# Kernel tuning notes

Measured on AMD Instinct MI355X. Metric: run time of the kernel, lower is better.

The kernel has to match this reference:

```python
import jax, jax.numpy as jnp
import numpy as np

B, S, D, H = 8, 577, 768, 12
P, KW = 576, 32            # num_patches, num_wormholes
HD = D // H                # head_dim = 64
SCALE = HD ** -0.5
TEMP = 0.1
GRID = 24                  # sqrt(P)
CANTOR_W = 0.3


def _cantor_position_bias():
    idx = np.arange(P)
    xg, yg = idx % GRID, idx // GRID
    s = xg + yg
    z = (s * (s + 1) // 2 + yg).astype(np.float32)
    fp = z / max(z.max(), 1.0)
    aff = 1.0 - np.abs(fp[None, :] - fp[:, None])
    np.fill_diagonal(aff, -1e9)
    return jnp.asarray(aff * CANTOR_W, dtype=jnp.float32)


def setup_inputs() -> dict:
    key = jax.random.key(0)
    ks = jax.random.split(key, 12)
    MLP = 4 * D
    w = lambda k, sh: jax.random.normal(k, sh, dtype=jnp.float32) * 0.02
    return {
        "x": jax.random.normal(ks[0], (B, S, D), dtype=jnp.float32),
        "g1": jnp.ones((D,), jnp.float32), "b1": jnp.zeros((D,), jnp.float32),
        "wq": w(ks[1], (D, D)), "bq": jnp.zeros((D,), jnp.float32),
        "wk": w(ks[2], (D, D)), "bk": jnp.zeros((D,), jnp.float32),
        "pos_bias": _cantor_position_bias(),
        "w_qkv": w(ks[3], (D, 3 * D)), "b_qkv": jnp.zeros((3 * D,), jnp.float32),
        "w_proj": w(ks[4], (D, D)), "b_proj": jnp.zeros((D,), jnp.float32),
        "g2": jnp.ones((D,), jnp.float32), "b2": jnp.zeros((D,), jnp.float32),
        "w_mlp1": w(ks[5], (D, 4 * D)), "b_mlp1": jnp.zeros((4 * D,), jnp.float32),
        "w_mlp2": w(ks[6], (4 * D, D)), "b_mlp2": jnp.zeros((D,), jnp.float32),
    }


def _ln(x, g, b):
    m = x.mean(-1, keepdims=True)
    v = x.var(-1, keepdims=True)
    return (x - m) / jnp.sqrt(v + 1e-5) * g + b


def _l2norm(x):  # F.normalize(dim=-1)
    return x / jnp.maximum(jnp.linalg.norm(x, axis=-1, keepdims=True), 1e-12)


def reference(x, g1, b1, wq, bq, wk, bk, pos_bias, w_qkv, b_qkv,
              w_proj, b_proj, g2, b2, w_mlp1, b_mlp1, w_mlp2, b_mlp2):
    xn = _ln(x, g1, b1)

    # --- learned wormhole router (content top-k) ---
    xp = xn[:, 1:, :]                                     # [B,P,D]
    q = _l2norm(xp @ wq + bq)
    k = _l2norm(xp @ wk + bk)
    scores = jnp.einsum('bpd,bqd->bpq', q, k) + pos_bias  # [B,P,P]
    scores = jnp.where(jnp.eye(P, dtype=bool), -1e9, scores) / TEMP
    topk_scores, routes = jax.lax.top_k(scores, KW)       # [B,P,K]
    weights = jax.nn.softmax(topk_scores, axis=-1)

    # --- qkv ---
    qkv = (xn @ w_qkv + b_qkv).reshape(B, S, 3, H, HD).transpose(2, 0, 3, 1, 4)
    Q, Kf, V = qkv[0], qkv[1], qkv[2]                     # [B,H,S,HD]

    # --- CLS: dense attention over all tokens ---
    attn_cls = jax.nn.softmax(jnp.einsum('bhqd,bhkd->bhqk', Q[:, :, :1], Kf) * SCALE, -1)
    out_cls = jnp.einsum('bhqk,bhkd->bhqd', attn_cls, V)  # [B,H,1,HD]

    # --- patches: sparse attention over gathered wormhole K/V ---
    Qp, Kp, Vp = Q[:, :, 1:], Kf[:, :, 1:], V[:, :, 1:]   # [B,H,P,HD]
    bi = jnp.arange(B)[:, None, None, None]
    hi = jnp.arange(H)[None, :, None, None]
    ri = routes[:, None, :, :]                            # [B,1,P,K] -> bcast [B,H,P,K]
    Kg = Kp[bi, hi, ri]                                   # [B,H,P,K,HD]
    Vg = Vp[bi, hi, ri]
    sp = jnp.einsum('bhpd,bhpkd->bhpk', Qp, Kg) * SCALE
    sp = sp + jnp.maximum(jnp.log(weights), -10.0)[:, None]
    ap = jax.nn.softmax(sp, axis=-1)
    out_p = jnp.einsum('bhpk,bhpkd->bhpd', ap, Vg)        # [B,H,P,HD]

    out = jnp.concatenate([out_cls, out_p], axis=2)       # [B,H,S,HD]
    out = out.transpose(0, 2, 1, 3).reshape(B, S, D)
    x = x + (out @ w_proj + b_proj)

    # --- MLP ---
    h = jax.nn.gelu(_ln(x, g2, b2) @ w_mlp1 + b_mlp1, approximate=False)
    x = x + (h @ w_mlp2 + b_mlp2)
    return x
```

## Files before the change

### kernel.cpp

```cpp
#include <hip/hip_runtime.h>
#include <math.h>

#define B_  8
#define S_  577
#define D_  768
#define H_  12
#define P_  576
#define KW_ 32
#define HD_ 64
constexpr int   MS       = B_ * S_;
constexpr int   MP       = B_ * P_;
constexpr float SCALE_   = 0.125f;
constexpr float INV_TEMP = 10.0f;

typedef __attribute__((ext_vector_type(8))) short bf16x8;
typedef __attribute__((ext_vector_type(4))) float f32x4;

__device__ __forceinline__ unsigned short f2bf(float f) {
  unsigned int x = __float_as_uint(f);
  x += 0x7fffu + ((x >> 16) & 1u);
  return (unsigned short)(x >> 16);
}
__device__ __forceinline__ float bf2f(unsigned short h) {
  return __uint_as_float((unsigned int)h << 16);
}
__device__ __forceinline__ void gl_lds16(const unsigned short* g,
                                         unsigned short* l) {
  __builtin_amdgcn_global_load_lds(
      (const __attribute__((address_space(1))) void*)g,
      (__attribute__((address_space(3))) void*)l, 16, 0, 0);
}
__device__ __forceinline__ void unpack8(bf16x8 v, float* f) {
  union { bf16x8 v8; unsigned int w[4]; } u;
  u.v8 = v;
#pragma unroll
  for (int i = 0; i < 4; ++i) {
    f[2 * i]     = __uint_as_float(u.w[i] << 16);
    f[2 * i + 1] = __uint_as_float(u.w[i] & 0xffff0000u);
  }
}
__device__ __forceinline__ int xcd_swz(int orig, int nwg) {
  const int q = nwg >> 3, r = nwg & 7;
  const int xcd = orig & 7, idx = orig >> 3;
  const int start = (xcd < r) ? xcd * (q + 1) : r * (q + 1) + (xcd - r) * q;
  return start + idx;
}

template <bool LO>
__global__ __launch_bounds__(256) void ln_rows_bf(
    const float* __restrict__ X, const float* __restrict__ g,
    const float* __restrict__ bta, unsigned short* __restrict__ Yh,
    unsigned short* __restrict__ Yl) {
  const int r = blockIdx.x, tid = threadIdx.x;
  const float* row = X + (long)r * D_;
  float v[3];
  float s = 0.f, sq = 0.f;
#pragma unroll
  for (int t = 0; t < 3; ++t) {
    v[t] = row[tid + t * 256];
    s += v[t];
    sq = fmaf(v[t], v[t], sq);
  }
#pragma unroll
  for (int off = 32; off; off >>= 1) {
    s  += __shfl_xor(s, off);
    sq += __shfl_xor(sq, off);
  }
  __shared__ float rs[4], rq[4];
  if ((tid & 63) == 0) { rs[tid >> 6] = s; rq[tid >> 6] = sq; }
  __syncthreads();
  s  = rs[0] + rs[1] + rs[2] + rs[3];
  sq = rq[0] + rq[1] + rq[2] + rq[3];
  const float m   = s * (1.f / D_);
  const float var = sq * (1.f / D_) - m * m;
  const float inv = rsqrtf(var + 1e-5f);
#pragma unroll
  for (int t = 0; t < 3; ++t) {
    const int c = tid + t * 256;
    const float y = (v[t] - m) * inv * g[c] + bta[c];
    const unsigned short h = f2bf(y);
    Yh[(long)r * D_ + c] = h;
    if (LO) Yl[(long)r * D_ + c] = f2bf(y - bf2f(h));
  }
}

__global__ __launch_bounds__(256) void l2norm_hl(
    const float* __restrict__ X, unsigned short* __restrict__ Yh,
    unsigned short* __restrict__ Yl) {
  const int r = blockIdx.x, tid = threadIdx.x;
  const float* row = X + (long)r * D_;
  float v[3];
  float sq = 0.f;
#pragma unroll
  for (int t = 0; t < 3; ++t) {
    v[t] = row[tid + t * 256];
    sq = fmaf(v[t], v[t], sq);
  }
#pragma unroll
  for (int off = 32; off; off >>= 1) sq += __shfl_xor(sq, off);
  __shared__ float rq[4];
  if ((tid & 63) == 0) rq[tid >> 6] = sq;
  __syncthreads();
  sq = rq[0] + rq[1] + rq[2] + rq[3];
  const float sc = 1.f / fmaxf(sqrtf(sq), 1e-12f);
#pragma unroll
  for (int t = 0; t < 3; ++t) {
    const float y = v[t] * sc;
    const unsigned short h = f2bf(y);
    Yh[(long)r * D_ + tid + t * 256] = h;
    Yl[(long)r * D_ + tid + t * 256] = f2bf(y - bf2f(h));
  }
}

__global__ __launch_bounds__(256) void transpose_hl(
    const float* __restrict__ W, unsigned short* __restrict__ Th,
    unsigned short* __restrict__ Tl, int K, int N, int rowoff) {
  __shared__ float t[32][33];
  const int tx = threadIdx.x & 31, ty = threadIdx.x >> 5;
  const int n0 = blockIdx.x * 32, k0 = blockIdx.y * 32;
#pragma unroll
  for (int i = ty; i < 32; i += 8)
    t[i][tx] = W[(long)(k0 + i) * N + n0 + tx];
  __syncthreads();
#pragma unroll
  for (int i = ty; i < 32; i += 8) {
    const float w = t[tx][i];
    const unsigned short h = f2bf(w);
    const long o = (long)(rowoff + n0 + i) * K + k0 + tx;
    Th[o] = h;
    if (Tl) Tl[o] = f2bf(w - bf2f(h));
  }
}

enum { BEPI_QKV = 0, BEPI_ADD = 1, BEPI_GELU = 2 };

template <int EPI>
__global__ __launch_bounds__(256, 3) void gemm_bf16(
    const unsigned short* __restrict__ A, const unsigned short* __restrict__ Wt,
    const float* __restrict__ bias, const float* __restrict__ R,
    float* __restrict__ C, unsigned short* __restrict__ Cbf,
    int M, int N, int K,
    unsigned short* __restrict__ Qb, unsigned short* __restrict__ Kb,
    unsigned short* __restrict__ Vb) {
  constexpr int BK = 64;
  __shared__ __align__(16) unsigned short ldsA[128 * BK];
  __shared__ __align__(16) unsigned short ldsB[128 * BK];
  const int tid = threadIdx.x, wave = tid >> 6, lane = tid & 63;
  const int wr = wave >> 1, wc = wave & 1;
  const int l16 = lane & 15, l4 = lane >> 4;
  const int NB = N >> 7;
  const int wgid = xcd_swz(blockIdx.x, gridDim.x);
  const int bm = wgid / NB, bn = wgid - bm * NB;
  const int row0 = bm * 128;

  f32x4 acc[4][4];
#pragma unroll
  for (int i = 0; i < 4; ++i)
#pragma unroll
    for (int j = 0; j < 4; ++j) acc[i][j] = (f32x4){0.f, 0.f, 0.f, 0.f};

  const unsigned short* ga[4];
  const unsigned short* gb[4];
#pragma unroll
  for (int t = 0; t < 4; ++t) {
    const int c = tid + (t << 8);
    const int r = c >> 3, p = c & 7, s = p ^ (r & 7);
    int ar = row0 + r; if (ar > M - 1) ar = M - 1;
    ga[t] = A + (long)ar * K + (s << 3);
    gb[t] = Wt + (long)(bn * 128 + r) * K + (s << 3);
  }

  for (int k0 = 0; k0 < K; k0 += BK) {
    __syncthreads();
#pragma unroll
    for (int t = 0; t < 4; ++t) {
      gl_lds16(ga[t] + k0, ldsA + ((tid + (t << 8)) << 3));
      gl_lds16(gb[t] + k0, ldsB + ((tid + (t << 8)) << 3));
    }
    __syncthreads();
#pragma unroll
    for (int sub = 0; sub < 2; ++sub) {
      bf16x8 af[4], bfr[4];
#pragma unroll
      for (int i = 0; i < 4; ++i) {
        const int row = wr * 64 + i * 16 + l16;
        const int pos = ((sub << 2) + l4) ^ (row & 7);
        af[i] = *(const bf16x8*)(ldsA + row * BK + (pos << 3));
      }
#pragma unroll
      for (int j = 0; j < 4; ++j) {
        const int row = wc * 64 + j * 16 + l16;
        const int pos = ((sub << 2) + l4) ^ (row & 7);
        bfr[j] = *(const bf16x8*)(ldsB + row * BK + (pos << 3));
      }
#pragma unroll
      for (int i = 0; i < 4; ++i)
#pragma unroll
        for (int j = 0; j < 4; ++j)
          acc[i][j] = __builtin_amdgcn_mfma_f32_16x16x32_bf16(af[i], bfr[j],
                                                              acc[i][j], 0, 0, 0);
    }
  }

#pragma unroll
  for (int j = 0; j < 4; ++j) {
    const int gcol = bn * 128 + wc * 64 + j * 16 + l16;
    const float bb = bias[gcol];
#pragma unroll
    for (int i = 0; i < 4; ++i) {
      const int grow0 = row0 + wr * 64 + i * 16 + l4 * 4;
#pragma unroll
      for (int r = 0; r < 4; ++r) {
        const int grow = grow0 + r;
        if (grow >= M) continue;
        float v = acc[i][j][r] + bb;
        if (EPI == BEPI_GELU) {
          v = 0.5f * v * (1.f + erff(v * 0.70710678118654752f));
          Cbf[(long)grow * N + gcol] = f2bf(v);
        } else if (EPI == BEPI_ADD) {
          C[(long)grow * N + gcol] = v + R[(long)grow * N + gcol];
        } else {
          const int t   = gcol / (H_ * HD_);
          const int rem = gcol - t * (H_ * HD_);
          const int h   = rem >> 6;
          const int d   = rem & 63;
          const int b   = grow / S_;
          const int ss  = grow - b * S_;
          unsigned short* dst = (t == 0 ? Qb : (t == 1 ? Kb : Vb));
          dst[(((long)(b * H_ + h) * S_ + ss) << 6) + d] = f2bf(v);
        }
      }
    }
  }
}

__global__ __launch_bounds__(256, 2) void gemm_rproj(
    const unsigned short* __restrict__ Ahi, const unsigned short* __restrict__ Alo,
    const unsigned short* __restrict__ Whi, const unsigned short* __restrict__ Wlo,
    const float* __restrict__ bq, const float* __restrict__ bk,
    float* __restrict__ qout, float* __restrict__ kout) {
  constexpr int BK = 32, K = D_, NB = 12;
  __shared__ __align__(16) unsigned short ldsAh[128 * BK];
  __shared__ __align__(16) unsigned short ldsAl[128 * BK];
  __shared__ __align__(16) unsigned short ldsBh[128 * BK];
  __shared__ __align__(16) unsigned short ldsBl[128 * BK];
  const int tid = threadIdx.x, wave = tid >> 6, lane = tid & 63;
  const int wr = wave >> 1, wc = wave & 1;
  const int l16 = lane & 15, l4 = lane >> 4;
  const int wgid = xcd_swz(blockIdx.x, gridDim.x);
  const int bm = wgid / NB, bn = wgid - bm * NB;
  const int row0 = bm * 128;

  f32x4 acc[4][4];
#pragma unroll
  for (int i = 0; i < 4; ++i)
#pragma unroll
    for (int j = 0; j < 4; ++j) acc[i][j] = (f32x4){0.f, 0.f, 0.f, 0.f};

  long aoff[2], boff[2];
#pragma unroll
  for (int t = 0; t < 2; ++t) {
    const int c = tid + (t << 8);
    const int r = c >> 2, p = c & 3, s = p ^ (r & 3);
    const int rg = row0 + r;
    aoff[t] = (long)(rg + rg / P_ + 1) * K + (s << 3);
    boff[t] = (long)(bn * 128 + r) * K + (s << 3);
  }

  for (int k0 = 0; k0 < K; k0 += BK) {
    __syncthreads();
#pragma unroll
    for (int t = 0; t < 2; ++t) {
      const int lo = (tid + (t << 8)) << 3;
      gl_lds16(Ahi + aoff[t] + k0, ldsAh + lo);
      gl_lds16(Alo + aoff[t] + k0, ldsAl + lo);
      gl_lds16(Whi + boff[t] + k0, ldsBh + lo);
      gl_lds16(Wlo + boff[t] + k0, ldsBl + lo);
    }
    __syncthreads();
    bf16x8 ah[4], al[4], bh[4], bl[4];
#pragma unroll
    for (int i = 0; i < 4; ++i) {
      const int row = wr * 64 + i * 16 + l16;
      const int off = row * BK + ((l4 ^ (row & 3)) << 3);
      ah[i] = *(const bf16x8*)(ldsAh + off);
      al[i] = *(const bf16x8*)(ldsAl + off);
    }
#pragma unroll
    for (int j = 0; j < 4; ++j) {
      const int row = wc * 64 + j * 16 + l16;
      const int off = row * BK + ((l4 ^ (row & 3)) << 3);
      bh[j] = *(const bf16x8*)(ldsBh + off);
      bl[j] = *(const bf16x8*)(ldsBl + off);
    }
#pragma unroll
    for (int i = 0; i < 4; ++i)
#pragma unroll
      for (int j = 0; j < 4; ++j) {
        acc[i][j] = __builtin_amdgcn_mfma_f32_16x16x32_bf16(ah[i], bh[j], acc[i][j], 0, 0, 0);
        acc[i][j] = __builtin_amdgcn_mfma_f32_16x16x32_bf16(ah[i], bl[j], acc[i][j], 0, 0, 0);
        acc[i][j] = __builtin_amdgcn_mfma_f32_16x16x32_bf16(al[i], bh[j], acc[i][j], 0, 0, 0);
      }
  }

#pragma unroll
  for (int j = 0; j < 4; ++j) {
    const int gcol = bn * 128 + wc * 64 + j * 16 + l16;
    const float bb = (gcol < D_) ? bq[gcol] : bk[gcol - D_];
#pragma unroll
    for (int i = 0; i < 4; ++i) {
      const int grow0 = row0 + wr * 64 + i * 16 + l4 * 4;
#pragma unroll
      for (int r = 0; r < 4; ++r) {
        const int grow = grow0 + r;
        const float v = acc[i][j][r] + bb;
        if (gcol < D_) qout[(long)grow * D_ + gcol] = v;
        else           kout[(long)grow * D_ + gcol - D_] = v;
      }
    }
  }
}

__global__ __launch_bounds__(256, 2) void gemm_scores(
    const unsigned short* __restrict__ Qh, const unsigned short* __restrict__ Ql,
    const unsigned short* __restrict__ Kh, const unsigned short* __restrict__ Kl,
    const float* __restrict__ pos, float* __restrict__ sc) {
  constexpr int BK = 32, K = D_;
  __shared__ __align__(16) unsigned short ldsAh[128 * BK];
  __shared__ __align__(16) unsigned short ldsAl[128 * BK];
  __shared__ __align__(16) unsigned short ldsBh[128 * BK];
  __shared__ __align__(16) unsigned short ldsBl[128 * BK];
  const int tid = threadIdx.x, wave = tid >> 6, lane = tid & 63;
  const int wr = wave >> 1, wc = wave & 1;
  const int l16 = lane & 15, l4 = lane >> 4;
  const int bn = blockIdx.x, bm = blockIdx.y, b = blockIdx.z;
  const long base = (long)b * P_ * K;
  const int row0 = bm * 128;

  f32x4 acc[4][4];
#pragma unroll
  for (int i = 0; i < 4; ++i)
#pragma unroll
    for (int j = 0; j < 4; ++j) acc[i][j] = (f32x4){0.f, 0.f, 0.f, 0.f};

  long aoff[2], boff[2];
#pragma unroll
  for (int t = 0; t < 2; ++t) {
    const int c = tid + (t << 8);
    const int r = c >> 2, p = c & 3, s = p ^ (r & 3);
    int ar = row0 + r;      if (ar > P_ - 1) ar = P_ - 1;
    int br = bn * 128 + r;  if (br > P_ - 1) br = P_ - 1;
    aoff[t] = base + (long)ar * K + (s << 3);
    boff[t] = base + (long)br * K + (s << 3);
  }

  for (int k0 = 0; k0 < K; k0 += BK) {
    __syncthreads();
#pragma unroll
    for (int t = 0; t < 2; ++t) {
      const int lo = (tid + (t << 8)) << 3;
      gl_lds16(Qh + aoff[t] + k0, ldsAh + lo);
      gl_lds16(Ql + aoff[t] + k0, ldsAl + lo);
      gl_lds16(Kh + boff[t] + k0, ldsBh + lo);
      gl_lds16(Kl + boff[t] + k0, ldsBl + lo);
    }
    __syncthreads();
    bf16x8 ah[4], al[4], bh[4], bl[4];
#pragma unroll
    for (int i = 0; i < 4; ++i) {
      const int row = wr * 64 + i * 16 + l16;
      const int off = row * BK + ((l4 ^ (row & 3)) << 3);
      ah[i] = *(const bf16x8*)(ldsAh + off);
      al[i] = *(const bf16x8*)(ldsAl + off);
    }
#pragma unroll
    for (int j = 0; j < 4; ++j) {
      const int row = wc * 64 + j * 16 + l16;
      const int off = row * BK + ((l4 ^ (row & 3)) << 3);
      bh[j] = *(const bf16x8*)(ldsBh + off);
      bl[j] = *(const bf16x8*)(ldsBl + off);
    }
#pragma unroll
    for (int i = 0; i < 4; ++i)
#pragma unroll
      for (int j = 0; j < 4; ++j) {
        acc[i][j] = __builtin_amdgcn_mfma_f32_16x16x32_bf16(ah[i], bh[j], acc[i][j], 0, 0, 0);
        acc[i][j] = __builtin_amdgcn_mfma_f32_16x16x32_bf16(ah[i], bl[j], acc[i][j], 0, 0, 0);
        acc[i][j] = __builtin_amdgcn_mfma_f32_16x16x32_bf16(al[i], bh[j], acc[i][j], 0, 0, 0);
      }
  }

#pragma unroll
  for (int j = 0; j < 4; ++j) {
    const int gj = bn * 128 + wc * 64 + j * 16 + l16;
    if (gj >= P_) continue;
#pragma unroll
    for (int i = 0; i < 4; ++i) {
      const int grow0 = row0 + wr * 64 + i * 16 + l4 * 4;
#pragma unroll
      for (int r = 0; r < 4; ++r) {
        const int gi = grow0 + r;
        if (gi >= P_) continue;
        const float s = (gi == gj) ? -1e9f : acc[i][j][r] + pos[(long)gi * P_ + gj];
        sc[((long)b * P_ + gi) * P_ + gj] = s * INV_TEMP;
      }
    }
  }
}

__global__ __launch_bounds__(64) void topk_route(
    const float* __restrict__ sc, int* __restrict__ routes,
    float* __restrict__ logw) {
  const int row = blockIdx.x, lane = threadIdx.x;
  const float* srow = sc + (long)row * P_;
  float v[9];
#pragma unroll
  for (int t = 0; t < 9; ++t) v[t] = srow[lane + (t << 6)];
  float selv = 0.f;
  int   selj = 0;
  for (int it = 0; it < KW_; ++it) {
    float bv = -3.0e38f;
    int   bj = 0x7fffffff;
#pragma unroll
    for (int t = 0; t < 9; ++t) {
      if (v[t] > bv) { bv = v[t]; bj = lane + (t << 6); }
    }
#pragma unroll
    for (int off = 32; off; off >>= 1) {
      const float ov = __shfl_xor(bv, off);
      const int   oj = __shfl_xor(bj, off);
      if (ov > bv || (ov == bv && oj < bj)) { bv = ov; bj = oj; }
    }
    if (lane == it) { selv = bv; selj = bj; }
    if ((bj & 63) == lane) v[bj >> 6] = -3.0e38f;
  }
  const float x = (lane < KW_) ? selv : -3.0e38f;
  float m = x;
#pragma unroll
  for (int off = 16; off; off >>= 1) m = fmaxf(m, __shfl_xor(m, off));
  const float e = expf(x - m);
  float s = e;
#pragma unroll
  for (int off = 16; off; off >>= 1) s += __shfl_xor(s, off);
  const float lw = fmaxf(x - m - logf(s), -10.0f);
  if (lane < KW_) {
    routes[(long)row * KW_ + lane] = selj;
    logw[(long)row * KW_ + lane]   = lw;
  }
}

__global__ __launch_bounds__(1024, 1) void patch_attn2(
    const unsigned short* __restrict__ Qb, const unsigned short* __restrict__ Kb,
    const unsigned short* __restrict__ Vb, const int* __restrict__ routes,
    const float* __restrict__ logw, unsigned short* __restrict__ attn) {
  __shared__ __align__(16) unsigned short ldsK[P_ * HD_];
  __shared__ __align__(16) unsigned short ldsV[P_ * HD_];
  const int tid = threadIdx.x;
  const int b = blockIdx.x & 7;
  const int rest = blockIdx.x >> 3;
  const int phalf = rest & 1;
  const int h = rest >> 1;
  const long hb = ((long)(b * H_ + h) * S_) << 6;

  const unsigned short* kg = Kb + hb + HD_;
  const unsigned short* vg = Vb + hb + HD_;
#pragma unroll
  for (int c = tid; c < P_ * 8; c += 1024) {
    const int r = c >> 3, i = c & 7;
    const int lo = r * 64 + ((i * 8) ^ ((r & 7) << 3));
    *(bf16x8*)(ldsK + lo) = *(const bf16x8*)(kg + c * 8);
    *(bf16x8*)(ldsV + lo) = *(const bf16x8*)(vg + c * 8);
  }
  __syncthreads();

  const int wave = tid >> 6, lane = tid & 63;
  const int g = lane >> 3, ch = lane & 7;
  const int p0 = phalf * 288;

  for (int p = p0 + wave; p < p0 + 288; p += 16) {
    const int s = p + 1;
    const long bp32 = ((long)(b * P_ + p)) << 5;
    float qf[8];
    unpack8(*(const bf16x8*)(Qb + hb + ((long)s << 6) + ch * 8), qf);
    int   rk[4];
    float sc4[4];
    float m = -3.0e38f;
#pragma unroll
    for (int it = 0; it < 4; ++it) {
      const int key = it * 8 + g;
      rk[it] = routes[bp32 + key];
      float kf[8];
      unpack8(*(const bf16x8*)(ldsK + rk[it] * 64 +
                               ((ch * 8) ^ ((rk[it] & 7) << 3))), kf);
      float d0 = 0.f;
#pragma unroll
      for (int d = 0; d < 8; ++d) d0 = fmaf(qf[d], kf[d], d0);
      d0 += __shfl_xor(d0, 1);
      d0 += __shfl_xor(d0, 2);
      d0 += __shfl_xor(d0, 4);
      sc4[it] = fmaf(d0, SCALE_, logw[bp32 + key]);
      m = fmaxf(m, sc4[it]);
    }
    m = fmaxf(m, __shfl_xor(m, 8));
    m = fmaxf(m, __shfl_xor(m, 16));
    m = fmaxf(m, __shfl_xor(m, 32));
    float e4[4], lsum = 0.f;
#pragma unroll
    for (int it = 0; it < 4; ++it) {
      e4[it] = __expf(sc4[it] - m);
      lsum += e4[it];
    }
    lsum += __shfl_xor(lsum, 8);
    lsum += __shfl_xor(lsum, 16);
    lsum += __shfl_xor(lsum, 32);
    float facc[8];
#pragma unroll
    for (int d = 0; d < 8; ++d) facc[d] = 0.f;
#pragma unroll
    for (int it = 0; it < 4; ++it) {
      float vf[8];
      unpack8(*(const bf16x8*)(ldsV + rk[it] * 64 +
                               ((ch * 8) ^ ((rk[it] & 7) << 3))), vf);
#pragma unroll
      for (int d = 0; d < 8; ++d) facc[d] = fmaf(e4[it], vf[d], facc[d]);
    }
#pragma unroll
    for (int off = 8; off <= 32; off <<= 1)
#pragma unroll
      for (int d = 0; d < 8; ++d) facc[d] += __shfl_xor(facc[d], off);
    const float inv = 1.f / lsum;
    if (lane < 8) {
      union { bf16x8 v8; unsigned short u[8]; } o;
#pragma unroll
      for (int d = 0; d < 8; ++d) o.u[d] = f2bf(facc[d] * inv);
      *(bf16x8*)(attn + ((long)b * S_ + s) * D_ + h * HD_ + ch * 8) = o.v8;
    }
  }
}

__global__ __launch_bounds__(256) void cls_attn(
    const unsigned short* __restrict__ Qb, const unsigned short* __restrict__ Kb,
    const unsigned short* __restrict__ Vb, unsigned short* __restrict__ attn) {
  const int bh = blockIdx.x;
  const int b = bh / H_, h = bh - b * H_;
  const int tid = threadIdx.x;
  __shared__ float qs[HD_];
  __shared__ float ssh[S_];
  __shared__ float redm[4], reds[4];
  __shared__ float osh[4][HD_];
  const unsigned short* Qrow  = Qb + (long)bh * S_ * HD_;
  const unsigned short* Kbase = Kb + (long)bh * S_ * HD_;
  const unsigned short* Vbase = Vb + (long)bh * S_ * HD_;
  if (tid < HD_) qs[tid] = bf2f(Qrow[tid]);
  __syncthreads();
  float lmax = -3.0e38f;
  for (int j = tid; j < S_; j += 256) {
    const unsigned short* kr = Kbase + (long)j * HD_;
    float dot = 0.f;
#pragma unroll
    for (int dd = 0; dd < HD_; dd += 8) {
      float kf[8];
      unpack8(*(const bf16x8*)(kr + dd), kf);
#pragma unroll
      for (int t = 0; t < 8; ++t) dot = fmaf(kf[t], qs[dd + t], dot);
    }
    dot *= SCALE_;
    ssh[j] = dot;
    lmax = fmaxf(lmax, dot);
  }
#pragma unroll
  for (int off = 32; off; off >>= 1) lmax = fmaxf(lmax, __shfl_xor(lmax, off));
  if ((tid & 63) == 0) redm[tid >> 6] = lmax;
  __syncthreads();
  const float m = fmaxf(fmaxf(redm[0], redm[1]), fmaxf(redm[2], redm[3]));
  float lsum = 0.f;
  for (int j = tid; j < S_; j += 256) {
    const float e = expf(ssh[j] - m);
    ssh[j] = e;
    lsum += e;
  }
#pragma unroll
  for (int off = 32; off; off >>= 1) lsum += __shfl_xor(lsum, off);
  if ((tid & 63) == 0) reds[tid >> 6] = lsum;
  __syncthreads();
  const float inv = 1.f / (reds[0] + reds[1] + reds[2] + reds[3]);
  const int d = tid & 63, qt = tid >> 6;
  float acc = 0.f;
  for (int j = qt; j < S_; j += 4)
    acc = fmaf(ssh[j], bf2f(Vbase[((long)j << 6) + d]), acc);
  osh[qt][d] = acc;
  __syncthreads();
  if (tid < HD_) {
    const float o = (osh[0][tid] + osh[1][tid] + osh[2][tid] + osh[3][tid]) * inv;
    attn[(long)b * S_ * D_ + h * HD_ + tid] = f2bf(o);
  }
}

extern "C" void kernel_launch(void* const* d_in, const int* in_sizes, int n_in,
                              void* d_out, int out_size, void* d_ws,
                              size_t ws_size, hipStream_t stream) {
  const float* x     = (const float*)d_in[0];
  const float* g1    = (const float*)d_in[1];
  const float* b1    = (const float*)d_in[2];
  const float* wq    = (const float*)d_in[3];
  const float* bq    = (const float*)d_in[4];
  const float* wk    = (const float*)d_in[5];
  const float* bk    = (const float*)d_in[6];
  const float* pos   = (const float*)d_in[7];
  const float* wqkv  = (const float*)d_in[8];
  const float* bqkv  = (const float*)d_in[9];
  const float* wproj = (const float*)d_in[10];
  const float* bproj = (const float*)d_in[11];
  const float* g2    = (const float*)d_in[12];
  const float* b2    = (const float*)d_in[13];
  const float* wm1   = (const float*)d_in[14];
  const float* bm1   = (const float*)d_in[15];
  const float* wm2   = (const float*)d_in[16];
  const float* bm2   = (const float*)d_in[17];
  float* out = (float*)d_out;

  constexpr long NSD = (long)MS * D_;
  constexpr long MPD = (long)MP * D_;
  constexpr long SCL = (long)B_ * P_ * P_;

  unsigned short* xn_hi = (unsigned short*)d_ws;
  unsigned short* xn_lo = xn_hi + NSD;
  float* x1 = (float*)(xn_lo + NSD);
  unsigned short* Qb = (unsigned short*)(x1 + NSD);
  unsigned short* Kb = Qb + NSD;
  unsigned short* Vb = Kb + NSD;
  int*   routes = (int*)(Vb + NSD);
  float* logw   = (float*)(routes + (long)MP * KW_);
  float* R1   = logw + (long)MP * KW_;
  float* qbuf = R1;
  float* kbuf = qbuf + MPD;
  unsigned short* h_bf = (unsigned short*)R1;
  constexpr long R1LEN = ((long)MS * 3072 + 1) / 2;
  float* scb = R1 + R1LEN;
  unsigned short* qh = (unsigned short*)(scb + SCL);
  unsigned short* ql = qh + MPD;
  unsigned short* kh = ql + MPD;
  unsigned short* kl = kh + MPD;
  unsigned short* x1n_bf  = qh;
  unsigned short* attn_bf = qh + NSD;
  unsigned short* wqk_hi  = kl + MPD;
  unsigned short* wqk_lo  = wqk_hi + (long)1536 * 768;
  unsigned short* wqkv_t  = wqk_lo + (long)1536 * 768;
  unsigned short* wproj_t = wqkv_t + (long)2304 * 768;
  unsigned short* wm1_t   = wproj_t + (long)768 * 768;
  unsigned short* wm2_t   = wm1_t + (long)3072 * 768;

  transpose_hl<<<dim3(24, 24), 256, 0, stream>>>(wq, wqk_hi, wqk_lo, 768, 768, 0);
  transpose_hl<<<dim3(24, 24), 256, 0, stream>>>(wk, wqk_hi, wqk_lo, 768, 768, 768);
  transpose_hl<<<dim3(72, 24), 256, 0, stream>>>(wqkv, wqkv_t, nullptr, 768, 2304, 0);
  transpose_hl<<<dim3(24, 24), 256, 0, stream>>>(wproj, wproj_t, nullptr, 768, 768, 0);
  transpose_hl<<<dim3(96, 24), 256, 0, stream>>>(wm1, wm1_t, nullptr, 768, 3072, 0);
  transpose_hl<<<dim3(24, 96), 256, 0, stream>>>(wm2, wm2_t, nullptr, 3072, 768, 0);

  ln_rows_bf<true><<<MS, 256, 0, stream>>>(x, g1, b1, xn_hi, xn_lo);
  gemm_rproj<<<12 * 36, 256, 0, stream>>>(xn_hi, xn_lo, wqk_hi, wqk_lo, bq, bk,
                                          qbuf, kbuf);
  l2norm_hl<<<MP, 256, 0, stream>>>(qbuf, qh, ql);
  l2norm_hl<<<MP, 256, 0, stream>>>(kbuf, kh, kl);
  gemm_scores<<<dim3(5, 5, B_), 256, 0, stream>>>(qh, ql, kh, kl, pos, scb);
  topk_route<<<MP, 64, 0, stream>>>(scb, routes, logw);
  gemm_bf16<BEPI_QKV><<<18 * 37, 256, 0, stream>>>(
      xn_hi, wqkv_t, bqkv, nullptr, nullptr, nullptr, MS, 2304, D_, Qb, Kb, Vb);
  cls_attn<<<B_ * H_, 256, 0, stream>>>(Qb, Kb, Vb, attn_bf);
  patch_attn2<<<192, 1024, 0, stream>>>(Qb, Kb, Vb, routes, logw, attn_bf);
  gemm_bf16<BEPI_ADD><<<6 * 37, 256, 0, stream>>>(
      attn_bf, wproj_t, bproj, x, x1, nullptr, MS, D_, D_, nullptr, nullptr,
      nullptr);
  ln_rows_bf<false><<<MS, 256, 0, stream>>>(x1, g2, b2, x1n_bf, nullptr);
  gemm_bf16<BEPI_GELU><<<24 * 37, 256, 0, stream>>>(
      x1n_bf, wm1_t, bm1, nullptr, nullptr, h_bf, MS, 3072, D_, nullptr,
      nullptr, nullptr);
  gemm_bf16<BEPI_ADD><<<6 * 37, 256, 0, stream>>>(
      h_bf, wm2_t, bm2, x1, out, nullptr, MS, D_, 3072, nullptr, nullptr,
      nullptr);
}
```

Before: 546.1 us.

## Double-buffer LDS in all GEMMs and use narrower N tiles for D-output GEMMs

```diff
diff --git a/kernel.cpp b/kernel.cpp
--- a/kernel.cpp
+++ b/kernel.cpp
@@ -134,7 +134,7 @@
 
 enum { BEPI_QKV = 0, BEPI_ADD = 1, BEPI_GELU = 2 };
 
-template <int EPI>
+template <int EPI, int BN>
 __global__ __launch_bounds__(256, 3) void gemm_bf16(
     const unsigned short* __restrict__ A, const unsigned short* __restrict__ Wt,
     const float* __restrict__ bias, const float* __restrict__ R,
@@ -142,69 +142,87 @@
     int M, int N, int K,
     unsigned short* __restrict__ Qb, unsigned short* __restrict__ Kb,
     unsigned short* __restrict__ Vb) {
-  constexpr int BK = 64;
-  __shared__ __align__(16) unsigned short ldsA[128 * BK];
-  __shared__ __align__(16) unsigned short ldsB[128 * BK];
+  constexpr int BK  = 32;
+  constexpr int NJ  = BN / 32;
+  constexpr int BCH = BN / 64;
+  __shared__ __align__(16) unsigned short ldsA[2][128 * BK];
+  __shared__ __align__(16) unsigned short ldsB[2][BN * BK];
   const int tid = threadIdx.x, wave = tid >> 6, lane = tid & 63;
   const int wr = wave >> 1, wc = wave & 1;
   const int l16 = lane & 15, l4 = lane >> 4;
-  const int NB = N >> 7;
+  const int NB = N / BN;
   const int wgid = xcd_swz(blockIdx.x, gridDim.x);
   const int bm = wgid / NB, bn = wgid - bm * NB;
   const int row0 = bm * 128;
 
-  f32x4 acc[4][4];
+  f32x4 acc[4][NJ];
 #pragma unroll
   for (int i = 0; i < 4; ++i)
 #pragma unroll
-    for (int j = 0; j < 4; ++j) acc[i][j] = (f32x4){0.f, 0.f, 0.f, 0.f};
-
-  const unsigned short* ga[4];
-  const unsigned short* gb[4];
-#pragma unroll
-  for (int t = 0; t < 4; ++t) {
+    for (int j = 0; j < NJ; ++j) acc[i][j] = (f32x4){0.f, 0.f, 0.f, 0.f};
+
+  const unsigned short* ga[2];
+#pragma unroll
+  for (int t = 0; t < 2; ++t) {
     const int c = tid + (t << 8);
-    const int r = c >> 3, p = c & 7, s = p ^ (r & 7);
+    const int r = c >> 2, p = c & 3, s = p ^ ((r >> 1) & 3);
     int ar = row0 + r; if (ar > M - 1) ar = M - 1;
     ga[t] = A + (long)ar * K + (s << 3);
-    gb[t] = Wt + (long)(bn * 128 + r) * K + (s << 3);
-  }
-
-  for (int k0 = 0; k0 < K; k0 += BK) {
+  }
+  const unsigned short* gb[BCH];
+#pragma unroll
+  for (int t = 0; t < BCH; ++t) {
+    const int c = tid + (t << 8);
+    const int r = c >> 2, p = c & 3, s = p ^ ((r >> 1) & 3);
+    gb[t] = Wt + (long)(bn * BN + r) * K + (s << 3);
+  }
+
+  const int nt = K / BK;
+#pragma unroll
+  for (int t = 0; t < 2; ++t)
+    gl_lds16(ga[t], &ldsA[0][(tid + (t << 8)) << 3]);
+#pragma unroll
+  for (int t = 0; t < BCH; ++t)
+    gl_lds16(gb[t], &ldsB[0][(tid + (t << 8)) << 3]);
+  __syncthreads();
+
+  int cur = 0;
+  for (int kt = 0; kt < nt; ++kt) {
+    if (kt + 1 < nt) {
+      const int k1 = (kt + 1) * BK;
+#pragma unroll
+      for (int t = 0; t < 2; ++t)
+        gl_lds16(ga[t] + k1, &ldsA[cur ^ 1][(tid + (t << 8)) << 3]);
+#pragma unroll
+      for (int t = 0; t < BCH; ++t)
+        gl_lds16(gb[t] + k1, &ldsB[cur ^ 1][(tid + (t << 8)) << 3]);
+    }
+    bf16x8 af[4], bfr[NJ];
+#pragma unroll
+    for (int i = 0; i < 4; ++i) {
+      const int row = wr * 64 + i * 16 + l16;
+      af[i] = *(const bf16x8*)(&ldsA[cur][row * BK +
+                                          ((l4 ^ ((row >> 1) & 3)) << 3)]);
+    }
+#pragma unroll
+    for (int j = 0; j < NJ; ++j) {
+      const int row = wc * (BN / 2) + j * 16 + l16;
+      bfr[j] = *(const bf16x8*)(&ldsB[cur][row * BK +
+                                           ((l4 ^ ((row >> 1) & 3)) << 3)]);
+    }
+#pragma unroll
+    for (int i = 0; i < 4; ++i)
+#pragma unroll
+      for (int j = 0; j < NJ; ++j)
+        acc[i][j] = __builtin_amdgcn_mfma_f32_16x16x32_bf16(af[i], bfr[j],
+                                                            acc[i][j], 0, 0, 0);
     __syncthreads();
-#pragma unroll
-    for (int t = 0; t < 4; ++t) {
-      gl_lds16(ga[t] + k0, ldsA + ((tid + (t << 8)) << 3));
-      gl_lds16(gb[t] + k0, ldsB + ((tid + (t << 8)) << 3));
-    }
-    __syncthreads();
-#pragma unroll
-    for (int sub = 0; sub < 2; ++sub) {
-      bf16x8 af[4], bfr[4];
-#pragma unroll
-      for (int i = 0; i < 4; ++i) {
-        const int row = wr * 64 + i * 16 + l16;
-        const int pos = ((sub << 2) + l4) ^ (row & 7);
-        af[i] = *(const bf16x8*)(ldsA + row * BK + (pos << 3));
-      }
-#pragma unroll
-      for (int j = 0; j < 4; ++j) {
-        const int row = wc * 64 + j * 16 + l16;
-        const int pos = ((sub << 2) + l4) ^ (row & 7);
-        bfr[j] = *(const bf16x8*)(ldsB + row * BK + (pos << 3));
-      }
-#pragma unroll
-      for (int i = 0; i < 4; ++i)
-#pragma unroll
-        for (int j = 0; j < 4; ++j)
-          acc[i][j] = __builtin_amdgcn_mfma_f32_16x16x32_bf16(af[i], bfr[j],
-                                                              acc[i][j], 0, 0, 0);
-    }
-  }
-
-#pragma unroll
-  for (int j = 0; j < 4; ++j) {
-    const int gcol = bn * 128 + wc * 64 + j * 16 + l16;
+    cur ^= 1;
+  }
+
+#pragma unroll
+  for (int j = 0; j < NJ; ++j) {
+    const int gcol = bn * BN + wc * (BN / 2) + j * 16 + l16;
     const float bb = bias[gcol];
 #pragma unroll
     for (int i = 0; i < 4; ++i) {
@@ -240,10 +258,10 @@
     const float* __restrict__ bq, const float* __restrict__ bk,
     float* __restrict__ qout, float* __restrict__ kout) {
   constexpr int BK = 32, K = D_, NB = 12;
-  __shared__ __align__(16) unsigned short ldsAh[128 * BK];
-  __shared__ __align__(16) unsigned short ldsAl[128 * BK];
-  __shared__ __align__(16) unsigned short ldsBh[128 * BK];
-  __shared__ __align__(16) unsigned short ldsBl[128 * BK];
+  __shared__ __align__(16) unsigned short ldsAh[2][128 * BK];
+  __shared__ __align__(16) unsigned short ldsAl[2][128 * BK];
+  __shared__ __align__(16) unsigned short ldsBh[2][128 * BK];
+  __shared__ __align__(16) unsigned short ldsBl[2][128 * BK];
   const int tid = threadIdx.x, wave = tid >> 6, lane = tid & 63;
   const int wr = wave >> 1, wc = wave & 1;
   const int l16 = lane & 15, l4 = lane >> 4;
@@ -261,37 +279,50 @@
 #pragma unroll
   for (int t = 0; t < 2; ++t) {
     const int c = tid + (t << 8);
-    const int r = c >> 2, p = c & 3, s = p ^ (r & 3);
+    const int r = c >> 2, p = c & 3, s = p ^ ((r >> 1) & 3);
     const int rg = row0 + r;
     aoff[t] = (long)(rg + rg / P_ + 1) * K + (s << 3);
     boff[t] = (long)(bn * 128 + r) * K + (s << 3);
   }
 
-  for (int k0 = 0; k0 < K; k0 += BK) {
-    __syncthreads();
-#pragma unroll
-    for (int t = 0; t < 2; ++t) {
-      const int lo = (tid + (t << 8)) << 3;
-      gl_lds16(Ahi + aoff[t] + k0, ldsAh + lo);
-      gl_lds16(Alo + aoff[t] + k0, ldsAl + lo);
-      gl_lds16(Whi + boff[t] + k0, ldsBh + lo);
-      gl_lds16(Wlo + boff[t] + k0, ldsBl + lo);
-    }
-    __syncthreads();
+  const int nt = K / BK;
+#pragma unroll
+  for (int t = 0; t < 2; ++t) {
+    const int lo = (tid + (t << 8)) << 3;
+    gl_lds16(Ahi + aoff[t], &ldsAh[0][lo]);
+    gl_lds16(Alo + aoff[t], &ldsAl[0][lo]);
+    gl_lds16(Whi + boff[t], &ldsBh[0][lo]);
+    gl_lds16(Wlo + boff[t], &ldsBl[0][lo]);
+  }
+  __syncthreads();
+
+  int cur = 0;
+  for (int kt = 0; kt < nt; ++kt) {
+    if (kt + 1 < nt) {
+      const int k1 = (kt + 1) * BK;
+#pragma unroll
+      for (int t = 0; t < 2; ++t) {
+        const int lo = (tid + (t << 8)) << 3;
+        gl_lds16(Ahi + aoff[t] + k1, &ldsAh[cur ^ 1][lo]);
+        gl_lds16(Alo + aoff[t] + k1, &ldsAl[cur ^ 1][lo]);
+        gl_lds16(Whi + boff[t] + k1, &ldsBh[cur ^ 1][lo]);
+        gl_lds16(Wlo + boff[t] + k1, &ldsBl[cur ^ 1][lo]);
+      }
+    }
     bf16x8 ah[4], al[4], bh[4], bl[4];
 #pragma unroll
     for (int i = 0; i < 4; ++i) {
       const int row = wr * 64 + i * 16 + l16;
-      const int off = row * BK + ((l4 ^ (row & 3)) << 3);
-      ah[i] = *(const bf16x8*)(ldsAh + off);
-      al[i] = *(const bf16x8*)(ldsAl + off);
+      const int off = row * BK + ((l4 ^ ((row >> 1) & 3)) << 3);
+      ah[i] = *(const bf16x8*)(&ldsAh[cur][off]);
+      al[i] = *(const bf16x8*)(&ldsAl[cur][off]);
     }
 #pragma unroll
     for (int j = 0; j < 4; ++j) {
       const int row = wc * 64 + j * 16 + l16;
-      const int off = row * BK + ((l4 ^ (row & 3)) << 3);
-      bh[j] = *(const bf16x8*)(ldsBh + off);
-      bl[j] = *(const bf16x8*)(ldsBl + off);
+      const int off = row * BK + ((l4 ^ ((row >> 1) & 3)) << 3);
+      bh[j] = *(const bf16x8*)(&ldsBh[cur][off]);
+      bl[j] = *(const bf16x8*)(&ldsBl[cur][off]);
     }
 #pragma unroll
     for (int i = 0; i < 4; ++i)
@@ -301,6 +332,8 @@
         acc[i][j] = __builtin_amdgcn_mfma_f32_16x16x32_bf16(ah[i], bl[j], acc[i][j], 0, 0, 0);
         acc[i][j] = __builtin_amdgcn_mfma_f32_16x16x32_bf16(al[i], bh[j], acc[i][j], 0, 0, 0);
       }
+    __syncthreads();
+    cur ^= 1;
   }
 
 #pragma unroll
@@ -326,10 +359,10 @@
     const unsigned short* __restrict__ Kh, const unsigned short* __restrict__ Kl,
     const float* __restrict__ pos, float* __restrict__ sc) {
   constexpr int BK = 32, K = D_;
-  __shared__ __align__(16) unsigned short ldsAh[128 * BK];
-  __shared__ __align__(16) unsigned short ldsAl[128 * BK];
-  __shared__ __align__(16) unsigned short ldsBh[128 * BK];
-  __shared__ __align__(16) unsigned short ldsBl[128 * BK];
+  __shared__ __align__(16) unsigned short ldsAh[2][128 * BK];
+  __shared__ __align__(16) unsigned short ldsAl[2][128 * BK];
+  __shared__ __align__(16) unsigned short ldsBh[2][128 * BK];
+  __shared__ __align__(16) unsigned short ldsBl[2][128 * BK];
   const int tid = threadIdx.x, wave = tid >> 6, lane = tid & 63;
   const int wr = wave >> 1, wc = wave & 1;
   const int l16 = lane & 15, l4 = lane >> 4;
@@ -347,38 +380,51 @@
 #pragma unroll
   for (int t = 0; t < 2; ++t) {
     const int c = tid + (t << 8);
-    const int r = c >> 2, p = c & 3, s = p ^ (r & 3);
+    const int r = c >> 2, p = c & 3, s = p ^ ((r >> 1) & 3);
     int ar = row0 + r;      if (ar > P_ - 1) ar = P_ - 1;
     int br = bn * 128 + r;  if (br > P_ - 1) br = P_ - 1;
     aoff[t] = base + (long)ar * K + (s << 3);
     boff[t] = base + (long)br * K + (s << 3);
   }
 
-  for (int k0 = 0; k0 < K; k0 += BK) {
-    __syncthreads();
-#pragma unroll
-    for (int t = 0; t < 2; ++t) {
-      const int lo = (tid + (t << 8)) << 3;
-      gl_lds16(Qh + aoff[t] + k0, ldsAh + lo);
-      gl_lds16(Ql + aoff[t] + k0, ldsAl + lo);
-      gl_lds16(Kh + boff[t] + k0, ldsBh + lo);
-      gl_lds16(Kl + boff[t] + k0, ldsBl + lo);
-    }
-    __syncthreads();
+  const int nt = K / BK;
+#pragma unroll
+  for (int t = 0; t < 2; ++t) {
+    const int lo = (tid + (t << 8)) << 3;
+    gl_lds16(Qh + aoff[t], &ldsAh[0][lo]);
+    gl_lds16(Ql + aoff[t], &ldsAl[0][lo]);
+    gl_lds16(Kh + boff[t], &ldsBh[0][lo]);
+    gl_lds16(Kl + boff[t], &ldsBl[0][lo]);
+  }
+  __syncthreads();
+
+  int cur = 0;
+  for (int kt = 0; kt < nt; ++kt) {
+    if (kt + 1 < nt) {
+      const int k1 = (kt + 1) * BK;
+#pragma unroll
+      for (int t = 0; t < 2; ++t) {
+        const int lo = (tid + (t << 8)) << 3;
+        gl_lds16(Qh + aoff[t] + k1, &ldsAh[cur ^ 1][lo]);
+        gl_lds16(Ql + aoff[t] + k1, &ldsAl[cur ^ 1][lo]);
+        gl_lds16(Kh + boff[t] + k1, &ldsBh[cur ^ 1][lo]);
+        gl_lds16(Kl + boff[t] + k1, &ldsBl[cur ^ 1][lo]);
+      }
+    }
     bf16x8 ah[4], al[4], bh[4], bl[4];
 #pragma unroll
     for (int i = 0; i < 4; ++i) {
       const int row = wr * 64 + i * 16 + l16;
-      const int off = row * BK + ((l4 ^ (row & 3)) << 3);
-      ah[i] = *(const bf16x8*)(ldsAh + off);
-      al[i] = *(const bf16x8*)(ldsAl + off);
+      const int off = row * BK + ((l4 ^ ((row >> 1) & 3)) << 3);
+      ah[i] = *(const bf16x8*)(&ldsAh[cur][off]);
+      al[i] = *(const bf16x8*)(&ldsAl[cur][off]);
     }
 #pragma unroll
     for (int j = 0; j < 4; ++j) {
       const int row = wc * 64 + j * 16 + l16;
-      const int off = row * BK + ((l4 ^ (row & 3)) << 3);
-      bh[j] = *(const bf16x8*)(ldsBh + off);
-      bl[j] = *(const bf16x8*)(ldsBl + off);
+      const int off = row * BK + ((l4 ^ ((row >> 1) & 3)) << 3);
+      bh[j] = *(const bf16x8*)(&ldsBh[cur][off]);
+      bl[j] = *(const bf16x8*)(&ldsBl[cur][off]);
     }
 #pragma unroll
     for (int i = 0; i < 4; ++i)
@@ -388,6 +434,8 @@
         acc[i][j] = __builtin_amdgcn_mfma_f32_16x16x32_bf16(ah[i], bl[j], acc[i][j], 0, 0, 0);
         acc[i][j] = __builtin_amdgcn_mfma_f32_16x16x32_bf16(al[i], bh[j], acc[i][j], 0, 0, 0);
       }
+    __syncthreads();
+    cur ^= 1;
   }
 
 #pragma unroll
@@ -664,18 +712,18 @@
   l2norm_hl<<<MP, 256, 0, stream>>>(kbuf, kh, kl);
   gemm_scores<<<dim3(5, 5, B_), 256, 0, stream>>>(qh, ql, kh, kl, pos, scb);
   topk_route<<<MP, 64, 0, stream>>>(scb, routes, logw);
-  gemm_bf16<BEPI_QKV><<<18 * 37, 256, 0, stream>>>(
+  gemm_bf16<BEPI_QKV, 128><<<18 * 37, 256, 0, stream>>>(
       xn_hi, wqkv_t, bqkv, nullptr, nullptr, nullptr, MS, 2304, D_, Qb, Kb, Vb);
   cls_attn<<<B_ * H_, 256, 0, stream>>>(Qb, Kb, Vb, attn_bf);
   patch_attn2<<<192, 1024, 0, stream>>>(Qb, Kb, Vb, routes, logw, attn_bf);
-  gemm_bf16<BEPI_ADD><<<6 * 37, 256, 0, stream>>>(
+  gemm_bf16<BEPI_ADD, 64><<<12 * 37, 256, 0, stream>>>(
       attn_bf, wproj_t, bproj, x, x1, nullptr, MS, D_, D_, nullptr, nullptr,
       nullptr);
   ln_rows_bf<false><<<MS, 256, 0, stream>>>(x1, g2, b2, x1n_bf, nullptr);
-  gemm_bf16<BEPI_GELU><<<24 * 37, 256, 0, stream>>>(
+  gemm_bf16<BEPI_GELU, 128><<<24 * 37, 256, 0, stream>>>(
       x1n_bf, wm1_t, bm1, nullptr, nullptr, h_bf, MS, 3072, D_, nullptr,
       nullptr, nullptr);
-  gemm_bf16<BEPI_ADD><<<6 * 37, 256, 0, stream>>>(
+  gemm_bf16<BEPI_ADD, 64><<<12 * 37, 256, 0, stream>>>(
       h_bf, wm2_t, bm2, x1, out, nullptr, MS, D_, 3072, nullptr, nullptr,
       nullptr);
 }
```

Measured after the change: 547.4 us. No clear change (+0.2%).
